# Kernel optimization log

Measured on AMD Instinct MI355X. Metric: run time of the kernel, lower is better.

The kernel has to match this reference:

```python
import jax, jax.numpy as jnp
import numpy as np

B, T, D, H = 4, 4096, 1024, 16
HD = D // H

def _phi(x):
    # ELU + 1 feature map (positive values)
    return jax.nn.elu(x) + 1.0

def setup_inputs() -> dict:
    key = jax.random.key(0)
    ks = jax.random.split(key, 6)
    s = D ** -0.5
    return {
        "x": jax.random.normal(ks[0], (B, T, D), dtype=jnp.float32),
        "mask": jax.random.randint(ks[1], (B, 1, 1, T), 0, 2).astype(bool),
        "Wq": jax.random.normal(ks[2], (D, D), dtype=jnp.float32) * s,
        "Wk": jax.random.normal(ks[3], (D, D), dtype=jnp.float32) * s,
        "Wv": jax.random.normal(ks[4], (D, D), dtype=jnp.float32) * s,
        "Wo": jax.random.normal(ks[5], (D, D), dtype=jnp.float32) * s,
    }

def reference(x, mask, Wq, Wk, Wv, Wo):
    b, t, d = x.shape
    def proj(W):
        # nn.Linear: y = x @ W.T ; split heads -> (B, H, T, HD)
        return (x @ W.T).reshape(b, t, H, HD).transpose(0, 2, 1, 3)
    q = _phi(proj(Wq))
    k = _phi(proj(Wk))
    v = proj(Wv)
    # mask.transpose(-2,-1): (B,1,1,T) -> (B,1,T,1); True positions zeroed
    m = jnp.swapaxes(mask, -2, -1)
    k = jnp.where(m, 0.0, k)
    v = jnp.where(m, 0.0, v)
    # kv = k^T v : (B,H,HD,HD) global pooling over T
    kv = jnp.einsum('bhtd,bhte->bhde', k, v)
    k_sum = k.sum(axis=-2)  # (B,H,HD)
    out = jnp.einsum('bhtd,bhde->bhte', q, kv)  # (B,H,T,HD)
    norm = jnp.maximum(jnp.einsum('bhtd,bhd->bht', q, k_sum)[..., None], 1e-6)
    out = (out / norm).transpose(0, 2, 1, 3).reshape(b, t, d)
    return out @ Wo.T  # dropout=0 (eval) -> identity
```

## Files before the change

### kernel.cpp

```cpp
#include <hip/hip_runtime.h>
#include <hip/hip_bf16.h>
#include <stdint.h>

#define T_ 4096
#define M_ 16384

typedef __attribute__((ext_vector_type(8))) short short8;
typedef __attribute__((ext_vector_type(4))) float f32x4;

__device__ __forceinline__ short f2b(float f) {
    __hip_bfloat16 h = __float2bfloat16(f);
    return __builtin_bit_cast(short, h);
}
__device__ __forceinline__ float b2f(short s) {
    unsigned int u = ((unsigned int)(unsigned short)s) << 16;
    return __builtin_bit_cast(float, u);
}
__device__ __forceinline__ void gload16(const void* g, void* l) {
    __builtin_amdgcn_global_load_lds(
        (const __attribute__((address_space(1))) void*)(unsigned long long)(uintptr_t)g,
        (__attribute__((address_space(3))) void*)(unsigned int)(uintptr_t)l,
        16, 0, 0);
}

__global__ __launch_bounds__(256) void cvt_x(const float* __restrict__ in,
                                             short* __restrict__ out) {
    long i = ((long)blockIdx.x * 256 + threadIdx.x) * 4;
    float4 f = *(const float4*)(in + i);
    short4 o; o.x = f2b(f.x); o.y = f2b(f.y); o.z = f2b(f.z); o.w = f2b(f.w);
    *(short4*)(out + i) = o;
}

__global__ __launch_bounds__(256) void cvt_weights(
    const float* __restrict__ Wq, const float* __restrict__ Wk,
    const float* __restrict__ Wv, const float* __restrict__ Wo,
    short* __restrict__ wqkvb, short* __restrict__ wob) {
    long i = ((long)blockIdx.x * 256 + threadIdx.x) * 4;
    int region = (int)(i >> 20);
    long off = i & 1048575;
    const float* src = region == 0 ? Wq : region == 1 ? Wk : region == 2 ? Wv : Wo;
    short* dst = region < 3 ? wqkvb + (long)region * 1048576 : wob;
    float4 f = *(const float4*)(src + off);
    short4 o; o.x = f2b(f.x); o.y = f2b(f.y); o.z = f2b(f.z); o.w = f2b(f.w);
    *(short4*)(dst + off) = o;
}

template <int MODE>
__global__ __launch_bounds__(512) void gemm8p(
    const short* __restrict__ A, const short* __restrict__ Bw,
    const int* __restrict__ mask,
    short* __restrict__ oQ, short* __restrict__ oK, short* __restrict__ oV,
    float* __restrict__ oF) {
    extern __shared__ short lds[];
    const int tid = threadIdx.x;
    const int wave = tid >> 6, lane = tid & 63;
    const int wm = wave >> 2, wn = wave & 3;

    const int nwg = gridDim.x;
    const int cpx = nwg >> 3;
    const int wg = (blockIdx.x & 7) * cpx + (blockIdx.x >> 3);
    const int bm = wg & 63, bn = wg >> 6;
    const long m0 = (long)bm * 256, n0 = (long)bn * 256;

    f32x4 acc[8][4];
#pragma unroll
    for (int i = 0; i < 8; ++i)
#pragma unroll
        for (int j = 0; j < 4; ++j) acc[i][j] = (f32x4)(0.0f);

    const short* aStageBase = A + (m0 + wave * 8 + (lane >> 3)) * 1024 +
                              (((lane & 7) ^ (lane >> 3)) * 8);
    const short* bStageBase = Bw + (n0 + wave * 8 + (lane >> 3)) * 1024 +
                              (((lane & 7) ^ (lane >> 3)) * 8);

    auto stage = [&](int t, int h, bool isA) {
        const short* src = (isA ? aStageBase : bStageBase) +
                           (long)(h * 128) * 1024 + t * 64;
        short* dst = lds + (isA ? 0 : 32768) + (t & 1) * 16384 + h * 8192 +
                     wave * 512;
        gload16(src, dst);
        gload16(src + 64 * 1024, dst + 4096);
    };

    const int laneR = lane & 15;
    const int sBase = (((lane >> 4) ^ (lane & 7)) * 8);

    short8 alo[4][2], ahi[4][2], blo[2][2], bhi[2][2];
    auto rdAlo = [&](int d) {
#pragma unroll
        for (int m = 0; m < 4; ++m)
#pragma unroll
            for (int kk = 0; kk < 2; ++kk)
                alo[m][kk] = *(const short8*)(lds + d * 16384 + wm * 8192 +
                                              (m * 16 + laneR) * 64 +
                                              (sBase ^ (kk * 32)));
    };
    auto rdAhi = [&](int d) {
#pragma unroll
        for (int m = 0; m < 4; ++m)
#pragma unroll
            for (int kk = 0; kk < 2; ++kk)
                ahi[m][kk] = *(const short8*)(lds + d * 16384 + wm * 8192 +
                                              ((m + 4) * 16 + laneR) * 64 +
                                              (sBase ^ (kk * 32)));
    };
    auto rdBlo = [&](int d) {
#pragma unroll
        for (int n = 0; n < 2; ++n)
#pragma unroll
            for (int kk = 0; kk < 2; ++kk)
                blo[n][kk] = *(const short8*)(lds + 32768 + d * 16384 +
                                              (wn >> 1) * 8192 +
                                              ((wn & 1) * 64 + n * 16 + laneR) * 64 +
                                              (sBase ^ (kk * 32)));
    };
    auto rdBhi = [&](int d) {
#pragma unroll
        for (int n = 0; n < 2; ++n)
#pragma unroll
            for (int kk = 0; kk < 2; ++kk)
                bhi[n][kk] = *(const short8*)(lds + 32768 + d * 16384 +
                                              (wn >> 1) * 8192 +
                                              ((wn & 1) * 64 + (n + 2) * 16 + laneR) * 64 +
                                              (sBase ^ (kk * 32)));
    };
    auto mm = [&](short8 (&a)[4][2], short8 (&b)[2][2], int mo, int no) {
        __builtin_amdgcn_s_setprio(1);
#pragma unroll
        for (int m = 0; m < 4; ++m)
#pragma unroll
            for (int n = 0; n < 2; ++n)
#pragma unroll
                for (int kk = 0; kk < 2; ++kk)
                    acc[mo + m][no + n] = __builtin_amdgcn_mfma_f32_16x16x32_bf16(
                        a[m][kk], b[n][kk], acc[mo + m][no + n], 0, 0, 0);
        __builtin_amdgcn_s_setprio(0);
    };

#define BAR()   __builtin_amdgcn_s_barrier()
#define LGKM0() asm volatile("s_waitcnt lgkmcnt(0)" ::: "memory")
#define VM4()   asm volatile("s_waitcnt vmcnt(4)" ::: "memory")
#define VM0()   asm volatile("s_waitcnt vmcnt(0)" ::: "memory")
#define SCHED0() __builtin_amdgcn_sched_barrier(0)

    stage(0, 0, true);  stage(0, 1, true);
    stage(0, 0, false); stage(0, 1, false);
    stage(1, 0, true);  stage(1, 1, true);
    VM4();
    BAR();

    for (int it = 0; it < 8; ++it) {
        const int t1 = 2 * it + 1, t2 = 2 * it + 2, t3 = 2 * it + 3;
        rdAlo(0); rdBlo(0);
        stage(t1, 0, false);
        BAR(); LGKM0();
        mm(alo, blo, 0, 0);
        BAR(); SCHED0();

        rdAhi(0); rdBhi(0);
        stage(t1, 1, false);
        BAR(); LGKM0();
        mm(ahi, bhi, 4, 2);
        BAR(); SCHED0();

        if (t2 < 16) stage(t2, 0, true);
        BAR();
        mm(ahi, blo, 4, 0);
        BAR(); SCHED0();

        if (t2 < 16) stage(t2, 1, true);
        if (it < 7) { VM4(); } else { VM0(); }
        BAR();
        mm(alo, bhi, 0, 2);
        BAR(); SCHED0();

        rdAlo(1); rdBlo(1);
        if (t2 < 16) stage(t2, 0, false);
        BAR(); LGKM0();
        mm(alo, blo, 0, 0);
        BAR(); SCHED0();

        rdAhi(1); rdBhi(1);
        if (t2 < 16) stage(t2, 1, false);
        BAR(); LGKM0();
        mm(ahi, bhi, 4, 2);
        BAR(); SCHED0();

        if (t3 < 16) stage(t3, 0, true);
        BAR();
        mm(ahi, blo, 4, 0);
        BAR(); SCHED0();

        if (t3 < 16) stage(t3, 1, true);
        if (it < 7) VM4();
        BAR();
        mm(alo, bhi, 0, 2);
        BAR(); SCHED0();
    }

    if (MODE == 0) {
        const int sec = (int)(n0 >> 10);
        short* outp = sec == 0 ? oQ : (sec == 1 ? oK : oV);
        const long cbase = n0 & 1023;
#pragma unroll
        for (int mi = 0; mi < 8; ++mi) {
#pragma unroll
            for (int r = 0; r < 4; ++r) {
                long gm = m0 + wm * 128 + mi * 16 + (lane >> 4) * 4 + r;
                int mz = (sec >= 1) ? mask[gm] : 0;
#pragma unroll
                for (int ni = 0; ni < 4; ++ni) {
                    long gn = cbase + wn * 64 + ni * 16 + (lane & 15);
                    float v = acc[mi][ni][r];
                    if (sec <= 1) v = (v > 0.f) ? v + 1.f : __expf(v);
                    if (mz) v = 0.f;
                    outp[gm * 1024 + gn] = f2b(v);
                }
            }
        }
    } else {
#pragma unroll
        for (int mi = 0; mi < 8; ++mi)
#pragma unroll
            for (int r = 0; r < 4; ++r) {
                long gm = m0 + wm * 128 + mi * 16 + (lane >> 4) * 4 + r;
#pragma unroll
                for (int ni = 0; ni < 4; ++ni) {
                    long gn = n0 + wn * 64 + ni * 16 + (lane & 15);
                    oF[gm * 1024 + gn] = acc[mi][ni][r];
                }
            }
    }
#undef BAR
#undef LGKM0
#undef VM4
#undef VM0
#undef SCHED0
}

__global__ __launch_bounds__(256) void kv_partial(
    const short* __restrict__ Kb, const short* __restrict__ Vb,
    float* __restrict__ kvp, float* __restrict__ ksp) {
    __shared__ __align__(16) float Ks[64][64];
    __shared__ __align__(16) float Vs[64][64];
    const int c = blockIdx.x, bh = blockIdx.y;
    const int b = bh >> 4, h = bh & 15;
    const int tid = threadIdx.x;
    const int dk = tid & 63, g = tid >> 6;
    float acc[16];
#pragma unroll
    for (int j = 0; j < 16; ++j) acc[j] = 0.f;
    float ks = 0.f;
    const long rowbase = (long)b * T_ + (long)c * 256;
    const int col0 = h * 64;

    for (int s = 0; s < 4; ++s) {
        __syncthreads();
        {
            int rr = tid >> 2;
            int cc = (tid & 3) * 16;
            const long gr = rowbase + s * 64 + rr;
            const short* kp = Kb + gr * 1024 + col0 + cc;
            const short* vp = Vb + gr * 1024 + col0 + cc;
            short8 k0 = *(const short8*)(kp);
            short8 k1 = *(const short8*)(kp + 8);
            short8 v0 = *(const short8*)(vp);
            short8 v1 = *(const short8*)(vp + 8);
            float kf[16], vf[16];
#pragma unroll
            for (int e = 0; e < 8; ++e) {
                kf[e] = b2f(k0[e]); kf[8 + e] = b2f(k1[e]);
                vf[e] = b2f(v0[e]); vf[8 + e] = b2f(v1[e]);
            }
#pragma unroll
            for (int q = 0; q < 4; ++q) {
                *(f32x4*)&Ks[rr][cc + q * 4] = *(f32x4*)&kf[q * 4];
                *(f32x4*)&Vs[rr][cc + q * 4] = *(f32x4*)&vf[q * 4];
            }
        }
        __syncthreads();
#pragma unroll 8
        for (int tt = 0; tt < 64; ++tt) {
            float kv_ = Ks[tt][dk];
            if (g == 0) ks += kv_;
            f32x4 v0 = *(const f32x4*)&Vs[tt][g * 16];
            f32x4 v1 = *(const f32x4*)&Vs[tt][g * 16 + 4];
            f32x4 v2 = *(const f32x4*)&Vs[tt][g * 16 + 8];
            f32x4 v3 = *(const f32x4*)&Vs[tt][g * 16 + 12];
#pragma unroll
            for (int e = 0; e < 4; ++e) {
                acc[e] += kv_ * v0[e];  acc[4 + e] += kv_ * v1[e];
                acc[8 + e] += kv_ * v2[e]; acc[12 + e] += kv_ * v3[e];
            }
        }
    }
    float* dst = kvp + ((long)bh * 16 + c) * 4096 + dk * 64 + g * 16;
#pragma unroll
    for (int q = 0; q < 4; ++q) *(f32x4*)(dst + q * 4) = *(f32x4*)&acc[q * 4];
    if (g == 0) ksp[((long)bh * 16 + c) * 64 + dk] = ks;
}

__global__ __launch_bounds__(256) void kv_reduce(
    const float* __restrict__ kvp, const float* __restrict__ ksp,
    short* __restrict__ kvT) {
    const int bh = blockIdx.x;
    const int tid = threadIdx.x;
    for (int e = tid; e < 4096; e += 256) {
        int dk = e >> 6, dv = e & 63;
        float s = 0.f;
#pragma unroll
        for (int c = 0; c < 16; ++c) s += kvp[((long)bh * 16 + c) * 4096 + e];
        kvT[(long)bh * 5120 + dv * 64 + dk] = f2b(s);
    }
    if (tid < 64) {
        float s = 0.f;
#pragma unroll
        for (int c = 0; c < 16; ++c) s += ksp[((long)bh * 16 + c) * 64 + tid];
        kvT[(long)bh * 5120 + 64 * 64 + tid] = f2b(s);
    }
    for (int e = tid; e < 15 * 64; e += 256)
        kvT[(long)bh * 5120 + 65 * 64 + e] = 0;
}

__global__ __launch_bounds__(256) void attn_out(
    const short* __restrict__ Qb, const short* __restrict__ kvT,
    short* __restrict__ attn) {
    __shared__ __align__(16) short Qs[128 * 64];
    const int tb = blockIdx.x, bh = blockIdx.y;
    const int b = bh >> 4, h = bh & 15;
    const int tid = threadIdx.x, wave = tid >> 6, lane = tid & 63;
    const long trow0 = (long)b * T_ + (long)tb * 128;
    const int col0 = h * 64;

    const int lr = lane >> 3, lc = (lane & 7) * 8;
    const short* qsrc = Qb + (trow0 + wave * 8 + lr) * 1024 + col0 + lc;
#pragma unroll
    for (int is = 0; is < 4; ++is)
        gload16(qsrc + (long)is * 32 * 1024, Qs + is * 2048 + wave * 512);

    short8 bfr[5][2];
    const short* kvb = kvT + (long)bh * 5120;
#pragma unroll
    for (int nf = 0; nf < 5; ++nf)
#pragma unroll
        for (int kk = 0; kk < 2; ++kk)
            bfr[nf][kk] = *(const short8*)(kvb + (nf * 16 + (lane & 15)) * 64 +
                                           kk * 32 + (lane >> 4) * 8);
    __syncthreads();

#pragma unroll
    for (int tf = 0; tf < 2; ++tf) {
        short8 af[2];
        int ar = wave * 32 + tf * 16 + (lane & 15);
#pragma unroll
        for (int kk = 0; kk < 2; ++kk)
            af[kk] = *(const short8*)(Qs + ar * 64 + kk * 32 + (lane >> 4) * 8);
        f32x4 oacc[5];
#pragma unroll
        for (int nf = 0; nf < 5; ++nf) {
            oacc[nf] = (f32x4)(0.0f);
#pragma unroll
            for (int kk = 0; kk < 2; ++kk)
                oacc[nf] = __builtin_amdgcn_mfma_f32_16x16x32_bf16(
                    af[kk], bfr[nf][kk], oacc[nf], 0, 0, 0);
        }
#pragma unroll
        for (int r = 0; r < 4; ++r) {
            float nv = __shfl(oacc[4][r], lane & 48, 64);
            nv = fmaxf(nv, 1e-6f);
            long gm = trow0 + wave * 32 + tf * 16 + (lane >> 4) * 4 + r;
#pragma unroll
            for (int nf = 0; nf < 4; ++nf) {
                float v = oacc[nf][r] / nv;
                attn[gm * 1024 + col0 + nf * 16 + (lane & 15)] = f2b(v);
            }
        }
    }
}

extern "C" void kernel_launch(void* const* d_in, const int* in_sizes, int n_in,
                              void* d_out, int out_size, void* d_ws, size_t ws_size,
                              hipStream_t stream) {
    const float* x = (const float*)d_in[0];
    const int* mask = (const int*)d_in[1];
    const float* Wq = (const float*)d_in[2];
    const float* Wk = (const float*)d_in[3];
    const float* Wv = (const float*)d_in[4];
    const float* Wo = (const float*)d_in[5];
    float* out = (float*)d_out;
    char* ws = (char*)d_ws;

    short* xb    = (short*)(ws);
    short* wqkvb = (short*)(ws + 33554432);
    short* wob   = (short*)(ws + 39845888);
    short* Qb    = (short*)(ws + 41943040);
    short* Kb    = (short*)(ws + 75497472);
    short* Vb    = (short*)(ws + 109051904);
    float* kvp   = (float*)(ws + 142606336);
    float* ksp   = (float*)(ws + 159383552);
    short* kvT   = (short*)(ws + 159645696);
    short* attnb = xb;

    static_assert(sizeof(void*) == 8, "");
    hipFuncSetAttribute((const void*)gemm8p<0>,
                        hipFuncAttributeMaxDynamicSharedMemorySize, 131072);
    hipFuncSetAttribute((const void*)gemm8p<1>,
                        hipFuncAttributeMaxDynamicSharedMemorySize, 131072);

    cvt_x<<<16384, 256, 0, stream>>>(x, xb);
    cvt_weights<<<4096, 256, 0, stream>>>(Wq, Wk, Wv, Wo, wqkvb, wob);
    gemm8p<0><<<768, 512, 131072, stream>>>(xb, wqkvb, mask, Qb, Kb, Vb, nullptr);
    kv_partial<<<dim3(16, 64), 256, 0, stream>>>(Kb, Vb, kvp, ksp);
    kv_reduce<<<64, 256, 0, stream>>>(kvp, ksp, kvT);
    attn_out<<<dim3(32, 64), 256, 0, stream>>>(Qb, kvT, attnb);
    gemm8p<1><<<256, 512, 131072, stream>>>(attnb, wob, nullptr, nullptr, nullptr,
                                            nullptr, out);
}
```

Baseline: 260.5 us.

## Replace 8-phase GEMM pipeline with simpler 4-stage per-k-tile schedule

Restructures the bf16 MFMA GEMM main loop from an 8-phase ping-pong schedule with partial vmcnt waits into a per-k-tile loop. Each loop iteration prefetches the next A and B tiles, runs four MFMA quadrants with interleaved LDS reads, and waits on vmcnt(0) at the end of the iteration. Staging is reorganised so each wave loads rows strided by 64 instead of half-tile blocks. The simpler schedule reduces barrier and phase bookkeeping, but it drains all global loads every k-step, which may expose more memory latency.

```diff
diff --git a/kernel.cpp b/kernel.cpp
--- a/kernel.cpp
+++ b/kernel.cpp
@@ -46,7 +46,7 @@
 }
 
 template <int MODE>
-__global__ __launch_bounds__(512) void gemm8p(
+__global__ __launch_bounds__(512) void gemm4s(
     const short* __restrict__ A, const short* __restrict__ Bw,
     const int* __restrict__ mask,
     short* __restrict__ oQ, short* __restrict__ oK, short* __restrict__ oV,
@@ -68,18 +68,27 @@
 #pragma unroll
         for (int j = 0; j < 4; ++j) acc[i][j] = (f32x4)(0.0f);
 
-    const short* aStageBase = A + (m0 + wave * 8 + (lane >> 3)) * 1024 +
+    const short* aStageBase = A + (m0 + (lane >> 3)) * 1024 +
                               (((lane & 7) ^ (lane >> 3)) * 8);
-    const short* bStageBase = Bw + (n0 + wave * 8 + (lane >> 3)) * 1024 +
+    const short* bStageBase = Bw + (n0 + (lane >> 3)) * 1024 +
                               (((lane & 7) ^ (lane >> 3)) * 8);
 
-    auto stage = [&](int t, int h, bool isA) {
-        const short* src = (isA ? aStageBase : bStageBase) +
-                           (long)(h * 128) * 1024 + t * 64;
-        short* dst = lds + (isA ? 0 : 32768) + (t & 1) * 16384 + h * 8192 +
-                     wave * 512;
-        gload16(src, dst);
-        gload16(src + 64 * 1024, dst + 4096);
+    auto stageA = [&](int t) {
+        const int d = t & 1;
+#pragma unroll
+        for (int j = 0; j < 4; ++j) {
+            const int r = wave * 8 + j * 64;
+            gload16(aStageBase + (long)r * 1024 + t * 64, lds + d * 16384 + r * 64);
+        }
+    };
+    auto stageB = [&](int t) {
+        const int d = t & 1;
+#pragma unroll
+        for (int j = 0; j < 4; ++j) {
+            const int r = wave * 8 + j * 64;
+            gload16(bStageBase + (long)r * 1024 + t * 64,
+                    lds + 32768 + d * 16384 + r * 64);
+        }
     };
 
     const int laneR = lane & 15;
@@ -137,64 +146,34 @@
         __builtin_amdgcn_s_setprio(0);
     };
 
-#define BAR()   __builtin_amdgcn_s_barrier()
-#define LGKM0() asm volatile("s_waitcnt lgkmcnt(0)" ::: "memory")
-#define VM4()   asm volatile("s_waitcnt vmcnt(4)" ::: "memory")
-#define VM0()   asm volatile("s_waitcnt vmcnt(0)" ::: "memory")
+#define BAR()    __builtin_amdgcn_s_barrier()
+#define LGKM0()  asm volatile("s_waitcnt lgkmcnt(0)" ::: "memory")
+#define VMW0()   asm volatile("s_waitcnt vmcnt(0)" ::: "memory")
 #define SCHED0() __builtin_amdgcn_sched_barrier(0)
 
-    stage(0, 0, true);  stage(0, 1, true);
-    stage(0, 0, false); stage(0, 1, false);
-    stage(1, 0, true);  stage(1, 1, true);
-    VM4();
+    stageA(0); stageB(0);
+    VMW0();
     BAR();
-
-    for (int it = 0; it < 8; ++it) {
-        const int t1 = 2 * it + 1, t2 = 2 * it + 2, t3 = 2 * it + 3;
-        rdAlo(0); rdBlo(0);
-        stage(t1, 0, false);
-        BAR(); LGKM0();
+    SCHED0();
+
+    for (int t = 0; t < 16; ++t) {
+        const int d = t & 1;
+        if (t + 1 < 16) stageA(t + 1);
+        rdAlo(d); rdBlo(d);
+        BAR(); LGKM0(); SCHED0();
         mm(alo, blo, 0, 0);
         BAR(); SCHED0();
-
-        rdAhi(0); rdBhi(0);
-        stage(t1, 1, false);
-        BAR(); LGKM0();
+        if (t + 1 < 16) stageB(t + 1);
+        rdAhi(d);
+        BAR(); LGKM0(); SCHED0();
+        mm(ahi, blo, 4, 0);
+        BAR(); SCHED0();
+        rdBhi(d);
+        BAR(); LGKM0(); SCHED0();
         mm(ahi, bhi, 4, 2);
         BAR(); SCHED0();
-
-        if (t2 < 16) stage(t2, 0, true);
-        BAR();
-        mm(ahi, blo, 4, 0);
-        BAR(); SCHED0();
-
-        if (t2 < 16) stage(t2, 1, true);
-        if (it < 7) { VM4(); } else { VM0(); }
-        BAR();
         mm(alo, bhi, 0, 2);
-        BAR(); SCHED0();
-
-        rdAlo(1); rdBlo(1);
-        if (t2 < 16) stage(t2, 0, false);
-        BAR(); LGKM0();
-        mm(alo, blo, 0, 0);
-        BAR(); SCHED0();
-
-        rdAhi(1); rdBhi(1);
-        if (t2 < 16) stage(t2, 1, false);
-        BAR(); LGKM0();
-        mm(ahi, bhi, 4, 2);
-        BAR(); SCHED0();
-
-        if (t3 < 16) stage(t3, 0, true);
-        BAR();
-        mm(ahi, blo, 4, 0);
-        BAR(); SCHED0();
-
-        if (t3 < 16) stage(t3, 1, true);
-        if (it < 7) VM4();
-        BAR();
-        mm(alo, bhi, 0, 2);
+        VMW0();
         BAR(); SCHED0();
     }
 
@@ -233,8 +212,7 @@
     }
 #undef BAR
 #undef LGKM0
-#undef VM4
-#undef VM0
+#undef VMW0
 #undef SCHED0
 }
 
@@ -401,18 +379,17 @@
     short* kvT   = (short*)(ws + 159645696);
     short* attnb = xb;
 
-    static_assert(sizeof(void*) == 8, "");
-    hipFuncSetAttribute((const void*)gemm8p<0>,
+    hipFuncSetAttribute((const void*)gemm4s<0>,
                         hipFuncAttributeMaxDynamicSharedMemorySize, 131072);
-    hipFuncSetAttribute((const void*)gemm8p<1>,
+    hipFuncSetAttribute((const void*)gemm4s<1>,
                         hipFuncAttributeMaxDynamicSharedMemorySize, 131072);
 
     cvt_x<<<16384, 256, 0, stream>>>(x, xb);
     cvt_weights<<<4096, 256, 0, stream>>>(Wq, Wk, Wv, Wo, wqkvb, wob);
-    gemm8p<0><<<768, 512, 131072, stream>>>(xb, wqkvb, mask, Qb, Kb, Vb, nullptr);
+    gemm4s<0><<<768, 512, 131072, stream>>>(xb, wqkvb, mask, Qb, Kb, Vb, nullptr);
     kv_partial<<<dim3(16, 64), 256, 0, stream>>>(Kb, Vb, kvp, ksp);
     kv_reduce<<<64, 256, 0, stream>>>(kvp, ksp, kvT);
     attn_out<<<dim3(32, 64), 256, 0, stream>>>(Qb, kvT, attnb);
-    gemm8p<1><<<256, 512, 131072, stream>>>(attnb, wob, nullptr, nullptr, nullptr,
+    gemm4s<1><<<256, 512, 131072, stream>>>(attnb, wob, nullptr, nullptr, nullptr,
                                             nullptr, out);
 }
```

Result: no change. 258.1 us (-0.9%).
